# Kernel optimization log

Hardware: AMD Instinct MI355X
Metric: run time of the kernel (lower is better)

Reference implementation:

```python
import jax, jax.numpy as jnp
import numpy as np

H = 16            # num heads
D_NOPE = 128
D_ROPE = 64
D_V = 128
Q_LORA = 1536
KV_LORA = 512
HIDDEN = 2048
EPS = 1e-6


def rmsnorm(x, w):
    xf = x.astype(jnp.float32)
    var = jnp.mean(xf * xf, axis=-1, keepdims=True)
    return (w * (xf * jax.lax.rsqrt(var + EPS))).astype(x.dtype)


def rope_interleaved(x, cos, sin):
    # x: [B,H,S,D]; cos,sin: [S,D] -> use even-index entries as the per-pair values
    B, nH, S, D = x.shape
    cv = cos[:, 0::2].astype(jnp.float32)[None, None]  # [1,1,S,D/2]
    sv = sin[:, 0::2].astype(jnp.float32)[None, None]
    xf = x.astype(jnp.float32).reshape(B, nH, S, D // 2, 2)
    xr, xi = xf[..., 0], xf[..., 1]
    out = jnp.stack([xr * cv - xi * sv, xr * sv + xi * cv], axis=-1)
    return out.reshape(B, nH, S, D).astype(x.dtype)


def setup_inputs() -> dict:
    key = jax.random.key(0)
    ks = jax.random.split(key, 9)
    B, S = 2, 2048
    std = 0.02
    return {
        "hidden_states": jax.random.normal(ks[0], (B, S, HIDDEN), jnp.float32),
        "cos": jax.random.uniform(ks[1], (S, D_ROPE), jnp.float32),
        "sin": jax.random.uniform(ks[2], (S, D_ROPE), jnp.float32),
        "q_a_w": jax.random.normal(ks[3], (HIDDEN, Q_LORA), jnp.float32) * std,
        "q_a_ln_w": jnp.ones((Q_LORA,), jnp.float32),
        "q_b_w": jax.random.normal(ks[4], (Q_LORA, H * (D_NOPE + D_ROPE)), jnp.float32) * std,
        "kv_a_w": jax.random.normal(ks[5], (HIDDEN, KV_LORA + D_ROPE), jnp.float32) * std,
        "kv_a_ln_w": jnp.ones((KV_LORA,), jnp.float32),
        "kv_b_w": jax.random.normal(ks[6], (KV_LORA, H * (D_NOPE + D_V)), jnp.float32) * std,
        "o_w": jax.random.normal(ks[7], (H * D_V, HIDDEN), jnp.float32) * std,
    }


def reference(hidden_states, cos, sin, q_a_w, q_a_ln_w, q_b_w, kv_a_w, kv_a_ln_w, kv_b_w, o_w):
    B, S, _ = hidden_states.shape
    scale = 1.0 / np.sqrt(D_NOPE + D_ROPE)

    # Q path: low-rank down-proj, RMSNorm, up-proj
    q = rmsnorm(hidden_states @ q_a_w, q_a_ln_w) @ q_b_w
    q = q.reshape(B, S, H, D_NOPE + D_ROPE).transpose(0, 2, 1, 3)  # [B,H,S,Dq]
    q_nope, q_rope = q[..., :D_NOPE], q[..., D_NOPE:]

    # KV path: compressed kv + shared rope key
    ckv = hidden_states @ kv_a_w  # [B,S,KV_LORA+D_ROPE]
    compressed_kv, k_rope = ckv[..., :KV_LORA], ckv[..., KV_LORA:]
    k_rope = jnp.broadcast_to(k_rope[:, None], (B, H, S, D_ROPE))
    kv = rmsnorm(compressed_kv, kv_a_ln_w) @ kv_b_w
    kv = kv.reshape(B, S, H, D_NOPE + D_V).transpose(0, 2, 1, 3)  # [B,H,S,Dk+Dv]
    k_nope, value = kv[..., :D_NOPE], kv[..., D_NOPE:]

    q_rope = rope_interleaved(q_rope, cos, sin)
    k_rope = rope_interleaved(k_rope, cos, sin)

    query = jnp.concatenate([q_nope, q_rope], axis=-1)  # [B,H,S,192]
    key = jnp.concatenate([k_nope, k_rope], axis=-1)

    attn = jnp.einsum("bhqd,bhkd->bhqk", query, key) * scale
    attn = jax.nn.softmax(attn.astype(jnp.float32), axis=-1).astype(query.dtype)
    out = jnp.einsum("bhqk,bhkd->bhqd", attn, value)  # [B,H,S,Dv]
    out = out.transpose(0, 2, 1, 3).reshape(B, S, H * D_V)
    return out @ o_w
```

## Files before the change

### kernel.cpp

```cpp
#include <hip/hip_runtime.h>

typedef unsigned short u16;
typedef __bf16 bf16x8 __attribute__((ext_vector_type(8)));
typedef float f32x4 __attribute__((ext_vector_type(4)));
typedef u16 u16x4 __attribute__((ext_vector_type(4)));

#define S_ 2048

__device__ __forceinline__ u16 f2bf(float f) {
  union { float f; unsigned u; } v; v.f = f;
  unsigned r = v.u + 0x7fffu + ((v.u >> 16) & 1u);
  return (u16)(r >> 16);
}
__device__ __forceinline__ float bf2f(u16 h) {
  union { unsigned u; float f; } v; v.u = ((unsigned)h) << 16;
  return v.f;
}

__device__ __forceinline__ f32x4 mfma16(bf16x8 a, bf16x8 b, f32x4 c) {
  return __builtin_amdgcn_mfma_f32_16x16x32_bf16(a, b, c, 0, 0, 0);
}

__device__ __forceinline__ void async16(const void* g, void* l) {
  __builtin_amdgcn_global_load_lds((__attribute__((address_space(1))) void*)g,
                                   (__attribute__((address_space(3))) void*)l,
                                   16, 0, 0);
}

__global__ void cast_bf8_k(const float* __restrict__ in, u16* __restrict__ out, int n8) {
  int i = blockIdx.x * 256 + threadIdx.x;
  if (i < n8) {
    f32x4 a = ((const f32x4*)in)[2 * i], b = ((const f32x4*)in)[2 * i + 1];
    union { u16 v[8]; f32x4 q; } u;
#pragma unroll
    for (int e = 0; e < 4; ++e) { u.v[e] = f2bf(a[e]); u.v[4 + e] = f2bf(b[e]); }
    ((f32x4*)out)[i] = u.q;
  }
}

__global__ void transw_k(const float* __restrict__ W, u16* __restrict__ Wt,
                         int K, int N) {
  __shared__ float tile[32][33];
  int k0 = blockIdx.x * 32, n0 = blockIdx.y * 32;
  int tx = threadIdx.x, ty = threadIdx.y;
#pragma unroll
  for (int r = 0; r < 32; r += 8) {
    int n = n0 + tx;
    tile[ty + r][tx] = (n < N) ? W[(long)(k0 + ty + r) * N + n] : 0.f;
  }
  __syncthreads();
#pragma unroll
  for (int r = 0; r < 32; r += 8) {
    Wt[(long)(n0 + ty + r) * K + k0 + tx] = f2bf(tile[tx][ty + r]);
  }
}

template <typename OUT_T, bool ROPE>
__global__ __launch_bounds__(256)
void gemm_bt_k(const u16* __restrict__ A, const u16* __restrict__ Bt,
               OUT_T* __restrict__ C, int K, int Nc, int ldc,
               const float* __restrict__ cs, const float* __restrict__ sn) {
  __shared__ __align__(16) u16 sA[128 * 32];
  __shared__ __align__(16) u16 sB[128 * 32];
  int tid = threadIdx.x;
  int lane = tid & 63, w = tid >> 6;
  int wr = w >> 1, wc = w & 1;
  int l15 = lane & 15, quad = lane >> 4;
  long tm = (long)blockIdx.y * 128;
  long tn = (long)blockIdx.x * 128;
  const u16* Ab = A + tm * K;
  const u16* Bb = Bt + tn * K;
  f32x4 acc[4][4] = {};

  for (int k0 = 0; k0 < K; k0 += 32) {
#pragma unroll
    for (int it = 0; it < 2; ++it) {
      int c = tid + it * 256;
      int row = c >> 2, kc = c & 3;
      async16(Ab + (long)row * K + k0 + kc * 8, sA + c * 8);
      async16(Bb + (long)row * K + k0 + kc * 8, sB + c * 8);
    }
    __syncthreads();
    bf16x8 af[4], bfr[4];
#pragma unroll
    for (int i = 0; i < 4; ++i)
      af[i] = *(const bf16x8*)(sA + (wr * 64 + i * 16 + l15) * 32 + quad * 8);
#pragma unroll
    for (int j = 0; j < 4; ++j)
      bfr[j] = *(const bf16x8*)(sB + (wc * 64 + j * 16 + l15) * 32 + quad * 8);
#pragma unroll
    for (int i = 0; i < 4; ++i)
#pragma unroll
      for (int j = 0; j < 4; ++j)
        acc[i][j] = mfma16(af[i], bfr[j], acc[i][j]);
    __syncthreads();
  }
#pragma unroll
  for (int i = 0; i < 4; ++i) {
#pragma unroll
    for (int j = 0; j < 4; ++j) {
      int col = (int)tn + wc * 64 + j * 16 + l15;
      if (col < Nc) {
        bool ropeT = false;
        int fi = 0;
        if constexpr (ROPE) {
          int d = col % 192;
          ropeT = (d >= 128);
          fi = (d - 128) & ~1;
        }
#pragma unroll
        for (int r = 0; r < 4; ++r) {
          long row = tm + wr * 64 + i * 16 + quad * 4 + r;
          float v = acc[i][j][r];
          if constexpr (ROPE) {
            float partner = __shfl_xor(v, 1);
            if (ropeT) {
              int si = (int)row & (S_ - 1);
              float cv = cs[si * 64 + fi], sv = sn[si * 64 + fi];
              v = (l15 & 1) ? (partner * sv + v * cv)
                            : (v * cv - partner * sv);
            }
          }
          if constexpr (sizeof(OUT_T) == 2) C[row * ldc + col] = f2bf(v);
          else                              C[row * ldc + col] = v;
        }
      }
    }
  }
}

__global__ __launch_bounds__(256)
void gemm_kvb_k(const u16* __restrict__ A, const u16* __restrict__ Bt,
                u16* __restrict__ kswz, u16* __restrict__ vswz) {
  const int K = 512;
  __shared__ __align__(16) u16 sA[128 * 32];
  __shared__ __align__(16) u16 sB[128 * 32];
  int tid = threadIdx.x;
  int lane = tid & 63, w = tid >> 6;
  int wr = w >> 1, wc = w & 1;
  int l15 = lane & 15, quad = lane >> 4;
  long tm = (long)blockIdx.y * 128;
  long tn = (long)blockIdx.x * 128;
  const u16* Ab = A + tm * K;
  const u16* Bb = Bt + tn * K;
  f32x4 acc[4][4] = {};

  for (int k0 = 0; k0 < K; k0 += 32) {
#pragma unroll
    for (int it = 0; it < 2; ++it) {
      int c = tid + it * 256;
      int row = c >> 2, kc = c & 3;
      async16(Ab + (long)row * K + k0 + kc * 8, sA + c * 8);
      async16(Bb + (long)row * K + k0 + kc * 8, sB + c * 8);
    }
    __syncthreads();
    bf16x8 af[4], bfr[4];
#pragma unroll
    for (int i = 0; i < 4; ++i)
      af[i] = *(const bf16x8*)(sA + (wr * 64 + i * 16 + l15) * 32 + quad * 8);
#pragma unroll
    for (int j = 0; j < 4; ++j)
      bfr[j] = *(const bf16x8*)(sB + (wc * 64 + j * 16 + l15) * 32 + quad * 8);
#pragma unroll
    for (int i = 0; i < 4; ++i)
#pragma unroll
      for (int j = 0; j < 4; ++j)
        acc[i][j] = mfma16(af[i], bfr[j], acc[i][j]);
    __syncthreads();
  }

  int h = (int)(tn >> 8);
  int b = (int)(tm >> 11);
  int tile = (b * 16 + h) * 32 + (((int)tm & 2047) >> 6) + wr;
  if ((tn & 255) == 0) {
    u16* dst = kswz + (long)tile * 12288;
#pragma unroll
    for (int i = 0; i < 4; ++i) {
#pragma unroll
      for (int j = 0; j < 4; ++j) {
        int frag = i * 6 + wc * 2 + (j >> 1);
        int chunk = frag * 64 + ((j & 1) * 2 + (l15 >> 3)) * 16 + quad * 4;
#pragma unroll
        for (int r = 0; r < 4; ++r)
          dst[(chunk + r) * 8 + (l15 & 7)] = f2bf(acc[i][j][r]);
      }
    }
  } else {
    u16* dst = vswz + (long)tile * 8192;
#pragma unroll
    for (int i = 0; i < 4; ++i) {
      int laneHi = ((i & 1) * 2 + (quad >> 1)) << 4;
      int kq = i >> 1;
      int e0 = (quad & 1) * 4;
#pragma unroll
      for (int j = 0; j < 4; ++j) {
        int frag = kq * 8 + wc * 4 + j;
        u16x4 pk;
#pragma unroll
        for (int r = 0; r < 4; ++r) pk[r] = f2bf(acc[i][j][r]);
        *(u16x4*)(dst + (frag * 64 + l15 + laneHi) * 8 + e0) = pk;
      }
    }
  }
}

__global__ __launch_bounds__(256)
void rmsnorm2_k(const float* __restrict__ qsrc, int ldq,
                const float* __restrict__ kvsrc, int ldkv,
                const float* __restrict__ wq, const float* __restrict__ wkv,
                u16* __restrict__ qout, u16* __restrict__ kvout) {
  int blk = blockIdx.x;
  const float* x; const float* wt; u16* o; int N;
  if (blk < 4096) { x = qsrc + (long)blk * ldq;  wt = wq;  o = qout + (long)blk * 1536;  N = 1536; }
  else { blk -= 4096; x = kvsrc + (long)blk * ldkv; wt = wkv; o = kvout + (long)blk * 512; N = 512; }
  float ss = 0.f;
  for (int i = threadIdx.x; i < N; i += 256) { float v = x[i]; ss += v * v; }
#pragma unroll
  for (int off = 32; off; off >>= 1) ss += __shfl_down(ss, off);
  __shared__ float red[4];
  if ((threadIdx.x & 63) == 0) red[threadIdx.x >> 6] = ss;
  __syncthreads();
  float inv = rsqrtf((red[0] + red[1] + red[2] + red[3]) / N + 1e-6f);
  for (int i = threadIdx.x; i < N; i += 256) o[i] = f2bf(wt[i] * x[i] * inv);
}

__global__ void krope_k(const float* __restrict__ src, int ld,
                        const float* __restrict__ cs, const float* __restrict__ sn,
                        u16* __restrict__ out) {
  int idx = blockIdx.x * 256 + threadIdx.x;
  int row = idx >> 5, i = idx & 31;
  int s = row & (S_ - 1);
  float xr = src[(long)row * ld + 2 * i];
  float xi = src[(long)row * ld + 2 * i + 1];
  float cv = cs[s * 64 + 2 * i], sv = sn[s * 64 + 2 * i];
  out[(long)row * 64 + 2 * i]     = f2bf(xr * cv - xi * sv);
  out[(long)row * 64 + 2 * i + 1] = f2bf(xr * sv + xi * cv);
}

__global__ void krfill_k(const u16* __restrict__ kr, u16* __restrict__ kswz) {
  int tile = blockIdx.x;
  int bh = tile >> 5, kt = tile & 31;
  int b = bh >> 4;
  u16* dst = kswz + (long)tile * 12288;
#pragma unroll
  for (int it = 0; it < 2; ++it) {
    int c = threadIdx.x + it * 256;
    int lane = c & 63, fd = c >> 6;
    int kg = fd >> 1, dbr = fd & 1;
    int key = kt * 64 + kg * 16 + (lane & 15);
    int doff = dbr * 32 + (lane >> 4) * 8;
    int frag = kg * 6 + 4 + dbr;
    *(f32x4*)(dst + (frag * 64 + lane) * 8) =
        *(const f32x4*)(kr + ((long)(b * S_ + key)) * 64 + doff);
  }
}

__global__ __launch_bounds__(256, 2)
void attn_k(const u16* __restrict__ qb, const u16* __restrict__ kswz,
            const u16* __restrict__ vswz, u16* __restrict__ attnO) {
  int bh = blockIdx.y, b = bh >> 4, h = bh & 15;
  int qt = blockIdx.x;
  int tid = threadIdx.x, lane = tid & 63, w = tid >> 6;
  int l15 = lane & 15, quad = lane >> 4;
  int qrow0 = qt * 128 + w * 32;

  __shared__ __align__(16) u16 sK[24 * 64 * 8];
  __shared__ __align__(16) u16 sV[16 * 64 * 8];
  __shared__ __align__(16) u16 pT[4][32 * 72];

  bf16x8 qf[2][6];
#pragma unroll
  for (int rg = 0; rg < 2; ++rg) {
    const u16* qp = qb + ((long)(b * S_ + qrow0 + rg * 16 + l15)) * 3072 + h * 192 + quad * 8;
#pragma unroll
    for (int kb = 0; kb < 6; ++kb) qf[rg][kb] = *(const bf16x8*)(qp + kb * 32);
  }

  f32x4 o[2][8] = {};
  float lsum[2][4] = {};
  u16* pw = pT[w];
  const float scale = 0.07216878364870322f;

#pragma unroll 1
  for (int kt = 0; kt < 32; ++kt) {
    const u16* Kt = kswz + ((long)bh * 32 + kt) * 12288;
    const u16* Vt = vswz + ((long)bh * 32 + kt) * 8192;
    __syncthreads();
#pragma unroll
    for (int i = 0; i < 6; ++i) {
      int c = tid + i * 256;
      async16(Kt + c * 8, sK + c * 8);
    }
#pragma unroll
    for (int i = 0; i < 4; ++i) {
      int c = tid + i * 256;
      async16(Vt + c * 8, sV + c * 8);
    }
    __syncthreads();

    f32x4 s[2][4] = {};
#pragma unroll
    for (int kg = 0; kg < 4; ++kg) {
#pragma unroll
      for (int db = 0; db < 6; ++db) {
        bf16x8 kf = *(const bf16x8*)(sK + ((kg * 6 + db) * 64 + lane) * 8);
        s[0][kg] = mfma16(qf[0][db], kf, s[0][kg]);
        s[1][kg] = mfma16(qf[1][db], kf, s[1][kg]);
      }
    }
#pragma unroll
    for (int rg = 0; rg < 2; ++rg) {
#pragma unroll
      for (int kg = 0; kg < 4; ++kg) {
#pragma unroll
        for (int r = 0; r < 4; ++r) {
          float p = __expf(s[rg][kg][r] * scale);
          lsum[rg][r] += p;
          pw[(rg * 16 + quad * 4 + r) * 72 + kg * 16 + l15] = f2bf(p);
        }
      }
    }
#pragma unroll
    for (int kq = 0; kq < 2; ++kq) {
      bf16x8 pf0 = *(const bf16x8*)(pw + (l15) * 72 + kq * 32 + quad * 8);
      bf16x8 pf1 = *(const bf16x8*)(pw + (16 + l15) * 72 + kq * 32 + quad * 8);
#pragma unroll
      for (int j = 0; j < 8; ++j) {
        bf16x8 vf = *(const bf16x8*)(sV + ((kq * 8 + j) * 64 + lane) * 8);
        o[0][j] = mfma16(pf0, vf, o[0][j]);
        o[1][j] = mfma16(pf1, vf, o[1][j]);
      }
    }
  }

  float inv[2][4];
#pragma unroll
  for (int rg = 0; rg < 2; ++rg)
#pragma unroll
    for (int r = 0; r < 4; ++r) {
      float s = lsum[rg][r];
#pragma unroll
      for (int off = 8; off; off >>= 1) s += __shfl_xor(s, off);
      inv[rg][r] = 1.f / s;
    }
#pragma unroll
  for (int rg = 0; rg < 2; ++rg) {
    u16* op = attnO + ((long)(b * S_ + qrow0 + rg * 16)) * 2048 + h * 128;
#pragma unroll
    for (int j = 0; j < 8; ++j)
#pragma unroll
      for (int r = 0; r < 4; ++r)
        op[(long)(quad * 4 + r) * 2048 + j * 16 + l15] = f2bf(o[rg][j][r] * inv[rg][r]);
  }
}

extern "C" void kernel_launch(void* const* d_in, const int* in_sizes, int n_in,
                              void* d_out, int out_size, void* d_ws, size_t ws_size,
                              hipStream_t stream) {
  const float* hs      = (const float*)d_in[0];
  const float* cosb    = (const float*)d_in[1];
  const float* sinb    = (const float*)d_in[2];
  const float* q_a_w   = (const float*)d_in[3];
  const float* q_a_ln  = (const float*)d_in[4];
  const float* q_b_w   = (const float*)d_in[5];
  const float* kv_a_w  = (const float*)d_in[6];
  const float* kv_a_ln = (const float*)d_in[7];
  const float* kv_b_w  = (const float*)d_in[8];
  const float* o_w     = (const float*)d_in[9];
  float* out = (float*)d_out;
  (void)in_sizes; (void)n_in; (void)out_size; (void)ws_size;

  char* p = (char*)d_ws;
  auto alloc = [&](size_t b) { char* r = p; p += (b + 255) & ~((size_t)255); return r; };
  u16*   hs_bf  = (u16*)  alloc((size_t)4096 * 2048 * 2);
  u16*   qakvT  = (u16*)  alloc((size_t)2176 * 2048 * 2);
  u16*   qbwT   = (u16*)  alloc((size_t)3072 * 1536 * 2);
  u16*   kvbwT  = (u16*)  alloc((size_t)4096 * 512  * 2);
  u16*   owT    = (u16*)  alloc((size_t)2048 * 2048 * 2);
  float* qa_ckv = (float*)alloc((size_t)4096 * 2176 * 4);
  u16*   qan    = (u16*)  alloc((size_t)4096 * 1536 * 2);
  u16*   ckvn   = (u16*)  alloc((size_t)4096 * 512  * 2);
  u16*   kr     = (u16*)  alloc((size_t)4096 * 64   * 2);
  u16*   qbuf   = (u16*)  alloc((size_t)4096 * 3072 * 2);
  u16*   aO     = (u16*)  alloc((size_t)4096 * 2048 * 2);
  u16* kswz = (u16*)qa_ckv;
  u16* vswz = (u16*)hs_bf;

  dim3 tb(32, 8);
  cast_bf8_k<<<4096, 256, 0, stream>>>(hs, hs_bf, 4096 * 2048 / 8);
  transw_k<<<dim3(64, 48),  tb, 0, stream>>>(q_a_w,  qakvT,                     2048, 1536);
  transw_k<<<dim3(64, 20),  tb, 0, stream>>>(kv_a_w, qakvT + (long)1536 * 2048, 2048, 576);
  transw_k<<<dim3(48, 96),  tb, 0, stream>>>(q_b_w,  qbwT,  1536, 3072);
  transw_k<<<dim3(16, 128), tb, 0, stream>>>(kv_b_w, kvbwT, 512,  4096);
  transw_k<<<dim3(64, 64),  tb, 0, stream>>>(o_w,    owT,   2048, 2048);

  gemm_bt_k<float, false><<<dim3(17, 32), 256, 0, stream>>>(
      hs_bf, qakvT, qa_ckv, 2048, 2176, 2176, nullptr, nullptr);
  rmsnorm2_k<<<8192, 256, 0, stream>>>(qa_ckv, 2176, qa_ckv + 1536, 2176,
                                       q_a_ln, kv_a_ln, qan, ckvn);
  krope_k<<<512, 256, 0, stream>>>(qa_ckv + 2048, 2176, cosb, sinb, kr);
  gemm_bt_k<u16, true><<<dim3(24, 32), 256, 0, stream>>>(
      qan, qbwT, qbuf, 1536, 3072, 3072, cosb, sinb);
  gemm_kvb_k<<<dim3(32, 32), 256, 0, stream>>>(ckvn, kvbwT, kswz, vswz);
  krfill_k<<<1024, 256, 0, stream>>>(kr, kswz);
  attn_k<<<dim3(16, 32), 256, 0, stream>>>(qbuf, kswz, vswz, aO);
  gemm_bt_k<float, false><<<dim3(16, 32), 256, 0, stream>>>(
      aO, owT, out, 2048, 2048, 2048, nullptr, nullptr);
}
```

Baseline: 502.5 us.

## Keep softmax probabilities in registers by transposing QK^T and permuting key layout

Swaps the MFMA operand order so the score tile comes out transposed, and permutes the key ordering in the swizzled K/V producers so each lane's exponentiated scores directly form a PV A-operand. This drops the per-wave LDS staging buffer for P along with its stores, loads and barriers, and packs P with v_cvt_pk_bf16_f32. Freeing that LDS lets the launch bound request three blocks per CU. The row-sum reduction becomes a shuffle across quads. The risk is a mismatch between the producer permutation and the consumer, and higher register pressure under the tighter occupancy bound.

```diff
diff --git a/kernel.cpp b/kernel.cpp
--- a/kernel.cpp
+++ b/kernel.cpp
@@ -178,8 +178,8 @@
     for (int i = 0; i < 4; ++i) {
 #pragma unroll
       for (int j = 0; j < 4; ++j) {
-        int frag = i * 6 + wc * 2 + (j >> 1);
-        int chunk = frag * 64 + ((j & 1) * 2 + (l15 >> 3)) * 16 + quad * 4;
+        int frag = quad * 6 + wc * 2 + (j >> 1);
+        int chunk = frag * 64 + ((j & 1) * 2 + (l15 >> 3)) * 16 + i * 4;
 #pragma unroll
         for (int r = 0; r < 4; ++r)
           dst[(chunk + r) * 8 + (l15 & 7)] = f2bf(acc[i][j][r]);
@@ -187,18 +187,17 @@
     }
   } else {
     u16* dst = vswz + (long)tile * 8192;
+    int kq = quad >> 1;
+    int e0 = (quad & 1) * 4;
 #pragma unroll
     for (int i = 0; i < 4; ++i) {
-      int laneHi = ((i & 1) * 2 + (quad >> 1)) << 4;
-      int kq = i >> 1;
-      int e0 = (quad & 1) * 4;
 #pragma unroll
       for (int j = 0; j < 4; ++j) {
         int frag = kq * 8 + wc * 4 + j;
         u16x4 pk;
 #pragma unroll
         for (int r = 0; r < 4; ++r) pk[r] = f2bf(acc[i][j][r]);
-        *(u16x4*)(dst + (frag * 64 + l15 + laneHi) * 8 + e0) = pk;
+        *(u16x4*)(dst + (frag * 64 + i * 16 + l15) * 8 + e0) = pk;
       }
     }
   }
@@ -247,7 +246,8 @@
     int c = threadIdx.x + it * 256;
     int lane = c & 63, fd = c >> 6;
     int kg = fd >> 1, dbr = fd & 1;
-    int key = kt * 64 + kg * 16 + (lane & 15);
+    int sl = lane & 15;
+    int key = kt * 64 + (sl >> 2) * 16 + kg * 4 + (sl & 3);
     int doff = dbr * 32 + (lane >> 4) * 8;
     int frag = kg * 6 + 4 + dbr;
     *(f32x4*)(dst + (frag * 64 + lane) * 8) =
@@ -255,7 +255,7 @@
   }
 }
 
-__global__ __launch_bounds__(256, 2)
+__global__ __launch_bounds__(256, 3)
 void attn_k(const u16* __restrict__ qb, const u16* __restrict__ kswz,
             const u16* __restrict__ vswz, u16* __restrict__ attnO) {
   int bh = blockIdx.y, b = bh >> 4, h = bh & 15;
@@ -266,7 +266,6 @@
 
   __shared__ __align__(16) u16 sK[24 * 64 * 8];
   __shared__ __align__(16) u16 sV[16 * 64 * 8];
-  __shared__ __align__(16) u16 pT[4][32 * 72];
 
   bf16x8 qf[2][6];
 #pragma unroll
@@ -277,8 +276,7 @@
   }
 
   f32x4 o[2][8] = {};
-  float lsum[2][4] = {};
-  u16* pw = pT[w];
+  float lsum[2] = {};
   const float scale = 0.07216878364870322f;
 
 #pragma unroll 1
@@ -304,10 +302,12 @@
 #pragma unroll
       for (int db = 0; db < 6; ++db) {
         bf16x8 kf = *(const bf16x8*)(sK + ((kg * 6 + db) * 64 + lane) * 8);
-        s[0][kg] = mfma16(qf[0][db], kf, s[0][kg]);
-        s[1][kg] = mfma16(qf[1][db], kf, s[1][kg]);
-      }
-    }
+        s[0][kg] = mfma16(kf, qf[0][db], s[0][kg]);
+        s[1][kg] = mfma16(kf, qf[1][db], s[1][kg]);
+      }
+    }
+
+    bf16x8 pf[2][2];
 #pragma unroll
     for (int rg = 0; rg < 2; ++rg) {
 #pragma unroll
@@ -315,34 +315,46 @@
 #pragma unroll
         for (int r = 0; r < 4; ++r) {
           float p = __expf(s[rg][kg][r] * scale);
-          lsum[rg][r] += p;
-          pw[(rg * 16 + quad * 4 + r) * 72 + kg * 16 + l15] = f2bf(p);
+          lsum[rg] += p;
+          s[rg][kg][r] = p;
         }
       }
-    }
+#pragma unroll
+      for (int kq = 0; kq < 2; ++kq) {
+        union { unsigned wd[4]; bf16x8 v; } u;
+        asm("v_cvt_pk_bf16_f32 %0, %1, %2"
+            : "=v"(u.wd[0]) : "v"(s[rg][2 * kq][0]), "v"(s[rg][2 * kq][1]));
+        asm("v_cvt_pk_bf16_f32 %0, %1, %2"
+            : "=v"(u.wd[1]) : "v"(s[rg][2 * kq][2]), "v"(s[rg][2 * kq][3]));
+        asm("v_cvt_pk_bf16_f32 %0, %1, %2"
+            : "=v"(u.wd[2]) : "v"(s[rg][2 * kq + 1][0]), "v"(s[rg][2 * kq + 1][1]));
+        asm("v_cvt_pk_bf16_f32 %0, %1, %2"
+            : "=v"(u.wd[3]) : "v"(s[rg][2 * kq + 1][2]), "v"(s[rg][2 * kq + 1][3]));
+        pf[rg][kq] = u.v;
+      }
+    }
+
 #pragma unroll
     for (int kq = 0; kq < 2; ++kq) {
-      bf16x8 pf0 = *(const bf16x8*)(pw + (l15) * 72 + kq * 32 + quad * 8);
-      bf16x8 pf1 = *(const bf16x8*)(pw + (16 + l15) * 72 + kq * 32 + quad * 8);
 #pragma unroll
       for (int j = 0; j < 8; ++j) {
         bf16x8 vf = *(const bf16x8*)(sV + ((kq * 8 + j) * 64 + lane) * 8);
-        o[0][j] = mfma16(pf0, vf, o[0][j]);
-        o[1][j] = mfma16(pf1, vf, o[1][j]);
-      }
-    }
-  }
-
-  float inv[2][4];
-#pragma unroll
-  for (int rg = 0; rg < 2; ++rg)
-#pragma unroll
-    for (int r = 0; r < 4; ++r) {
-      float s = lsum[rg][r];
-#pragma unroll
-      for (int off = 8; off; off >>= 1) s += __shfl_xor(s, off);
-      inv[rg][r] = 1.f / s;
-    }
+        o[0][j] = mfma16(pf[0][kq], vf, o[0][j]);
+        o[1][j] = mfma16(pf[1][kq], vf, o[1][j]);
+      }
+    }
+  }
+
+  float invr[2][4];
+#pragma unroll
+  for (int rg = 0; rg < 2; ++rg) {
+    float ssum = lsum[rg];
+    ssum += __shfl_xor(ssum, 16);
+    ssum += __shfl_xor(ssum, 32);
+#pragma unroll
+    for (int r = 0; r < 4; ++r)
+      invr[rg][r] = 1.f / __shfl(ssum, quad * 4 + r);
+  }
 #pragma unroll
   for (int rg = 0; rg < 2; ++rg) {
     u16* op = attnO + ((long)(b * S_ + qrow0 + rg * 16)) * 2048 + h * 128;
@@ -350,7 +362,7 @@
     for (int j = 0; j < 8; ++j)
 #pragma unroll
       for (int r = 0; r < 4; ++r)
-        op[(long)(quad * 4 + r) * 2048 + j * 16 + l15] = f2bf(o[rg][j][r] * inv[rg][r]);
+        op[(long)(quad * 4 + r) * 2048 + j * 16 + l15] = f2bf(o[rg][j][r] * invr[rg][r]);
   }
 }
 
```

After: 510.5 us. About the same (+1.6%).
